# Kernel tuning notes

Measured on AMD Instinct MI355X. Metric: run time of the kernel, lower is better.

## Reference

```python
import jax, jax.numpy as jnp
import numpy as np

N_NODES = 100000
N_EDGES = 1600000
IN_CH = 128
HID = 128
OUT_CH = 64
N_GRAPHS = 256


def setup_inputs() -> dict:
    key = jax.random.key(0)
    ks = jax.random.split(key, 12)
    x = jax.random.normal(ks[0], (N_NODES, IN_CH), dtype=jnp.float32)
    edge_index = jax.random.randint(ks[1], (2, N_EDGES), 0, N_NODES, dtype=jnp.int64)
    batch = jnp.sort(jax.random.randint(ks[2], (N_NODES,), 0, N_GRAPHS, dtype=jnp.int64))
    def glorot(k, shape):
        lim = np.sqrt(6.0 / (shape[0] + shape[1]))
        return jax.random.uniform(k, shape, jnp.float32, -lim, lim)
    w1 = glorot(ks[3], (IN_CH, HID)); b1 = jnp.zeros((HID,), jnp.float32)
    w2 = glorot(ks[4], (HID, HID));   b2 = jnp.zeros((HID,), jnp.float32)
    w3 = glorot(ks[5], (HID, HID));   b3 = jnp.zeros((HID,), jnp.float32)
    w_out = glorot(ks[6], (HID, OUT_CH)); b_out = jnp.zeros((OUT_CH,), jnp.float32)
    return {"x": x, "edge_index": edge_index, "batch": batch,
            "w1": w1, "b1": b1, "w2": w2, "b2": b2, "w3": w3, "b3": b3,
            "w_out": w_out, "b_out": b_out}


def reference(x, edge_index, batch, w1, b1, w2, b2, w3, b3, w_out, b_out):
    N = x.shape[0]
    # GCN normalization with added self-loops (PyG gcn_norm, symmetric):
    loop = jnp.arange(N, dtype=edge_index.dtype)
    src = jnp.concatenate([edge_index[0], loop])  # message source
    dst = jnp.concatenate([edge_index[1], loop])  # aggregate at target
    deg = jax.ops.segment_sum(jnp.ones(src.shape, jnp.float32), dst, num_segments=N)
    dinv = jax.lax.rsqrt(jnp.maximum(deg, 1.0))  # deg >= 1 due to self-loops
    norm = dinv[src] * dinv[dst]  # [E+N]

    def gcn_conv(h, w, b):
        h = h @ w  # transform first (PyG order)
        agg = jax.ops.segment_sum(norm[:, None] * h[src], dst, num_segments=N)
        return agg + b

    # norm module is None, dropout p=0 -> act-only branch, dropout no-op
    h = jax.nn.relu(gcn_conv(x, w1, b1))
    h = jax.nn.relu(gcn_conv(h, w2, b2))
    h = jax.nn.relu(gcn_conv(h, w3, b3))

    # global mean pool over graphs
    cnt = jax.ops.segment_sum(jnp.ones((N,), jnp.float32), batch, num_segments=N_GRAPHS)
    pooled = jax.ops.segment_sum(h, batch, num_segments=N_GRAPHS) / jnp.maximum(cnt, 1.0)[:, None]
    return pooled @ w_out + b_out  # [N_GRAPHS, OUT_CH]
```

## Files before the change

### kernel.cpp

```cpp
#include <hip/hip_runtime.h>
#include <hip/hip_fp16.h>

#define N_NODES 100000
#define N_EDGES 1600000
#define HID 128
#define OUT_CH 64
#define N_GRAPHS 256
#define CHUNK 1024
#define NCHUNK ((N_NODES + CHUNK - 1) / CHUNK)
#define NSLICE 8
#define SLICE_NODES ((N_NODES + NSLICE - 1) / NSLICE)
#define CAPB 262144
#define EPW2 1600

typedef _Float16 half8 __attribute__((ext_vector_type(8)));
typedef float f32x4 __attribute__((ext_vector_type(4)));

__global__ void k_setup(int* cnt, int* bcur, float* pooled, float* gcnt,
                        const float* __restrict__ w1, const float* __restrict__ w2,
                        const float* __restrict__ w3,
                        __half* __restrict__ wt1, __half* __restrict__ wt2,
                        __half* __restrict__ wt3) {
  int i = blockIdx.x * blockDim.x + threadIdx.x;
  int stride = gridDim.x * blockDim.x;
  for (int t = i; t < N_NODES; t += stride) cnt[t] = 0;
  for (int t = i; t < NSLICE; t += stride) bcur[t] = t * CAPB;
  for (int t = i; t < N_GRAPHS * HID; t += stride) pooled[t] = 0.f;
  for (int t = i; t < N_GRAPHS; t += stride) gcnt[t] = 0.f;
  for (int t = i; t < HID * HID; t += stride) {
    int n = t >> 7, k = t & 127;
    wt1[t] = __float2half(w1[k * HID + n]);
    wt2[t] = __float2half(w2[k * HID + n]);
    wt3[t] = __float2half(w3[k * HID + n]);
  }
}

__global__ __launch_bounds__(256) void k_part(const int* __restrict__ ei,
                                              int* __restrict__ bcur,
                                              int* __restrict__ bsrc,
                                              int* __restrict__ bdst) {
  __shared__ int hist[NSLICE], rbase[NSLICE], lcur[NSLICE];
  int tid = threadIdx.x;
  int e0 = blockIdx.x * EPW2;
  int n = min(EPW2, N_EDGES - e0);
  if (n <= 0) return;
  if (tid < NSLICE) { hist[tid] = 0; lcur[tid] = 0; }
  __syncthreads();
  for (int i = tid; i < n; i += 256)
    atomicAdd(&hist[ei[N_EDGES + e0 + i] / SLICE_NODES], 1);
  __syncthreads();
  if (tid < NSLICE) rbase[tid] = atomicAdd(&bcur[tid], hist[tid]);
  __syncthreads();
  for (int i = tid; i < n; i += 256) {
    int s = ei[e0 + i], d = ei[N_EDGES + e0 + i];
    int b = d / SLICE_NODES;
    int p = rbase[b] + atomicAdd(&lcur[b], 1);
    bsrc[p] = s;
    bdst[p] = d;
  }
}

__global__ __launch_bounds__(256) void k_count2(const int* __restrict__ bdst,
                                                const int* __restrict__ bcur,
                                                int* __restrict__ cnt) {
  int b = blockIdx.x & (NSLICE - 1);
  int base = b * CAPB;
  int sz = bcur[b] - base;
  int bi = blockIdx.x >> 3;
  int step = (gridDim.x >> 3) * 256;
  for (int i = bi * 256 + threadIdx.x; i < sz; i += step)
    atomicAdd(&cnt[bdst[base + i]], 1);
}

__global__ void k_scan1(const int* __restrict__ cnt, int* __restrict__ row_ptr,
                        int* __restrict__ chunk_sums) {
  __shared__ int s[CHUNK];
  int t = threadIdx.x;
  int gid = blockIdx.x * CHUNK + t;
  int v = (gid < N_NODES) ? cnt[gid] : 0;
  s[t] = v;
  __syncthreads();
  for (int off = 1; off < CHUNK; off <<= 1) {
    int add = (t >= off) ? s[t - off] : 0;
    __syncthreads();
    s[t] += add;
    __syncthreads();
  }
  if (gid < N_NODES) row_ptr[gid] = s[t] - v;
  if (t == CHUNK - 1) chunk_sums[blockIdx.x] = s[t];
}

__global__ void k_scan2(const int* __restrict__ chunk_sums, int* __restrict__ chunk_off) {
  __shared__ int s[128];
  int t = threadIdx.x;
  int v = (t < NCHUNK) ? chunk_sums[t] : 0;
  s[t] = v;
  __syncthreads();
  for (int off = 1; off < 128; off <<= 1) {
    int add = (t >= off) ? s[t - off] : 0;
    __syncthreads();
    s[t] += add;
    __syncthreads();
  }
  if (t < NCHUNK) chunk_off[t] = s[t] - v;
}

__global__ void k_scan3(int* __restrict__ row_ptr, const int* __restrict__ chunk_off,
                        int* __restrict__ cursor, const int* __restrict__ cnt,
                        float* __restrict__ dinv) {
  int i = blockIdx.x * blockDim.x + threadIdx.x;
  if (i < N_NODES) {
    int v = row_ptr[i] + chunk_off[i / CHUNK];
    row_ptr[i] = v;
    cursor[i] = v;
    dinv[i] = rsqrtf((float)cnt[i] + 1.0f);
  }
  if (i == 0) row_ptr[N_NODES] = N_EDGES;
}

__global__ __launch_bounds__(256) void k_fill2(const int* __restrict__ bsrc,
                                               const int* __restrict__ bdst,
                                               const int* __restrict__ bcur,
                                               int* __restrict__ cursor,
                                               int* __restrict__ E4) {
  int b = blockIdx.x & (NSLICE - 1);
  int base = b * CAPB;
  int sz = bcur[b] - base;
  int bi = blockIdx.x >> 3;
  int step = (gridDim.x >> 3) * 256;
  for (int i = bi * 256 + threadIdx.x; i < sz; i += step) {
    int d = bdst[base + i];
    int p = atomicAdd(&cursor[d], 1);
    E4[p] = bsrc[base + i];
  }
}

#define GBM 128
template <bool FP16IN>
__global__ __launch_bounds__(512) void k_gemm(const void* __restrict__ Hv,
                                              const __half* __restrict__ WT,
                                              __half* __restrict__ T) {
  __shared__ __half hs[GBM * HID];
  __shared__ __half ws[HID * HID];
  int tid = threadIdx.x;
  int m0 = blockIdx.x * GBM;

  for (int g = tid; g < GBM * 16; g += 512) {
    int r = g >> 4, kg = g & 15;
    int row = m0 + r;
    half8 h = {};
    if (row < N_NODES) {
      if constexpr (FP16IN) {
        h = *(const half8*)&((const _Float16*)Hv)[(size_t)row * HID + kg * 8];
      } else {
        const float* H = (const float*)Hv;
        float4 f0 = *(const float4*)&H[(size_t)row * HID + kg * 8];
        float4 f1 = *(const float4*)&H[(size_t)row * HID + kg * 8 + 4];
        h[0] = (_Float16)f0.x; h[1] = (_Float16)f0.y; h[2] = (_Float16)f0.z; h[3] = (_Float16)f0.w;
        h[4] = (_Float16)f1.x; h[5] = (_Float16)f1.y; h[6] = (_Float16)f1.z; h[7] = (_Float16)f1.w;
      }
    }
    int byte = (r * HID + kg * 8) * 2;
    byte ^= (r & 7) << 4;
    *(half8*)((char*)hs + byte) = h;
  }
  for (int g = tid; g < HID * 16; g += 512) {
    int n = g >> 4, kg = g & 15;
    half8 h = *(const half8*)&WT[n * HID + kg * 8];
    int byte = (n * HID + kg * 8) * 2;
    byte ^= (n & 7) << 4;
    *(half8*)((char*)ws + byte) = h;
  }
  __syncthreads();

  int w = tid >> 6, l = tid & 63;
  int r = (w << 4) + (l & 15);
  int kq = (l >> 4) << 3;
  f32x4 acc[8] = {};

  #pragma unroll
  for (int kc = 0; kc < HID; kc += 32) {
    int abyte = ((r * HID + kc + kq) * 2) ^ ((r & 7) << 4);
    half8 a = *(const half8*)((char*)hs + abyte);
    #pragma unroll
    for (int nb = 0; nb < 8; ++nb) {
      int n = nb * 16 + (l & 15);
      int bbyte = ((n * HID + kc + kq) * 2) ^ ((n & 7) << 4);
      half8 bfr = *(const half8*)((char*)ws + bbyte);
      acc[nb] = __builtin_amdgcn_mfma_f32_16x16x32_f16(a, bfr, acc[nb], 0, 0, 0);
    }
  }

  __syncthreads();
  #pragma unroll
  for (int nb = 0; nb < 8; ++nb) {
    #pragma unroll
    for (int j = 0; j < 4; ++j) {
      int rr = (w << 4) + ((l >> 4) << 2) + j;
      int cc = nb * 16 + (l & 15);
      int byte = (rr * HID + cc) * 2;
      byte ^= (rr & 7) << 4;
      *(__half*)((char*)hs + byte) = __float2half(acc[nb][j]);
    }
  }
  __syncthreads();
  for (int g = tid; g < GBM * 16; g += 512) {
    int rr = g >> 4, kg = g & 15;
    int byte = (rr * HID + kg * 8) * 2;
    byte ^= (rr & 7) << 4;
    half8 v = *(half8*)((char*)hs + byte);
    int row = m0 + rr;
    if (row < N_NODES)
      *(half8*)&((_Float16*)T)[(size_t)row * HID + kg * 8] = v;
  }
}

__device__ __forceinline__ void acc8(float* acc, uint4 v, float wt) {
  __half2 h0 = *(__half2*)&v.x, h1 = *(__half2*)&v.y;
  __half2 h2 = *(__half2*)&v.z, h3 = *(__half2*)&v.w;
  float2 f0 = __half22float2(h0), f1 = __half22float2(h1);
  float2 f2 = __half22float2(h2), f3 = __half22float2(h3);
  acc[0] += wt * f0.x; acc[1] += wt * f0.y;
  acc[2] += wt * f1.x; acc[3] += wt * f1.y;
  acc[4] += wt * f2.x; acc[5] += wt * f2.y;
  acc[6] += wt * f3.x; acc[7] += wt * f3.y;
}

__global__ __launch_bounds__(256) void k_agg(const __half* __restrict__ T,
                                             const int* __restrict__ row_ptr,
                                             const int* __restrict__ E4,
                                             const float* __restrict__ dinv,
                                             const float* __restrict__ bias,
                                             __half* __restrict__ Hout) {
  int wid = (blockIdx.x * blockDim.x + threadIdx.x) >> 6;
  int lane = threadIdx.x & 63;
  if (wid >= N_NODES) return;
  int q = lane >> 4;
  int wch = lane & 15;

  float acc[8] = {};
  float dn = dinv[wid];
  {
    uint4 vs = *(const uint4*)(T + (size_t)wid * HID + wch * 8);
    acc8(acc, vs, (q == 0) ? dn * dn : 0.f);
  }
  int p0 = row_ptr[wid], p1 = row_ptr[wid + 1];
  for (int p = p0; p < p1; p += 16) {
    int i0 = p + q, i1 = p + 4 + q, i2 = p + 8 + q, i3 = p + 12 + q;
    int c0 = min(i0, p1 - 1), c1 = min(i1, p1 - 1);
    int c2 = min(i2, p1 - 1), c3 = min(i3, p1 - 1);
    int s0 = E4[c0], s1 = E4[c1], s2 = E4[c2], s3 = E4[c3];
    uint4 v0 = *(const uint4*)(T + (size_t)s0 * HID + wch * 8);
    uint4 v1 = *(const uint4*)(T + (size_t)s1 * HID + wch * 8);
    uint4 v2 = *(const uint4*)(T + (size_t)s2 * HID + wch * 8);
    uint4 v3 = *(const uint4*)(T + (size_t)s3 * HID + wch * 8);
    float w0 = (i0 < p1) ? dinv[s0] * dn : 0.f;
    float w1 = (i1 < p1) ? dinv[s1] * dn : 0.f;
    float w2 = (i2 < p1) ? dinv[s2] * dn : 0.f;
    float w3 = (i3 < p1) ? dinv[s3] * dn : 0.f;
    acc8(acc, v0, w0);
    acc8(acc, v1, w1);
    acc8(acc, v2, w2);
    acc8(acc, v3, w3);
  }
  #pragma unroll
  for (int j = 0; j < 8; ++j) {
    acc[j] += __shfl_xor(acc[j], 16, 64);
    acc[j] += __shfl_xor(acc[j], 32, 64);
  }
  if (q == 0) {
    float4 b0 = *(const float4*)(bias + wch * 8);
    float4 b1 = *(const float4*)(bias + wch * 8 + 4);
    __half2 o0 = __floats2half2_rn(fmaxf(acc[0] + b0.x, 0.f), fmaxf(acc[1] + b0.y, 0.f));
    __half2 o1 = __floats2half2_rn(fmaxf(acc[2] + b0.z, 0.f), fmaxf(acc[3] + b0.w, 0.f));
    __half2 o2 = __floats2half2_rn(fmaxf(acc[4] + b1.x, 0.f), fmaxf(acc[5] + b1.y, 0.f));
    __half2 o3 = __floats2half2_rn(fmaxf(acc[6] + b1.z, 0.f), fmaxf(acc[7] + b1.w, 0.f));
    uint4 o;
    o.x = *(unsigned int*)&o0; o.y = *(unsigned int*)&o1;
    o.z = *(unsigned int*)&o2; o.w = *(unsigned int*)&o3;
    *(uint4*)(Hout + (size_t)wid * HID + wch * 8) = o;
  }
}

#define POOL_NODES 64
__global__ __launch_bounds__(256) void k_pool(const __half* __restrict__ H,
                                              const int* __restrict__ batch,
                                              float* __restrict__ pooled,
                                              float* __restrict__ gcnt) {
  int w = threadIdx.x >> 6;
  int l = threadIdx.x & 63;
  int n0 = blockIdx.x * POOL_NODES + w * 16;
  if (n0 >= N_NODES) return;
  int n1 = min(n0 + 16, N_NODES);
  const __half2* H2 = (const __half2*)H;
  float sx = 0.f, sy = 0.f, cntr = 0.f;
  int cur = batch[n0];
  for (int n = n0; n < n1; ++n) {
    int g = batch[n];
    if (g != cur) {
      atomicAdd(&pooled[cur * HID + 2 * l], sx);
      atomicAdd(&pooled[cur * HID + 2 * l + 1], sy);
      if (l == 0) atomicAdd(&gcnt[cur], cntr);
      sx = 0.f; sy = 0.f; cntr = 0.f; cur = g;
    }
    float2 f = __half22float2(H2[(size_t)n * 64 + l]);
    sx += f.x; sy += f.y; cntr += 1.f;
  }
  atomicAdd(&pooled[cur * HID + 2 * l], sx);
  atomicAdd(&pooled[cur * HID + 2 * l + 1], sy);
  if (l == 0) atomicAdd(&gcnt[cur], cntr);
}

__global__ __launch_bounds__(64) void k_out(const float* __restrict__ pooled,
                                            const float* __restrict__ gcnt,
                                            const float* __restrict__ w_out,
                                            const float* __restrict__ b_out,
                                            float* __restrict__ out) {
  int g = blockIdx.x;
  int c = threadIdx.x;
  __shared__ float p[HID];
  float inv = 1.0f / fmaxf(gcnt[g], 1.0f);
  for (int k = c; k < HID; k += 64) p[k] = pooled[g * HID + k] * inv;
  __syncthreads();
  float acc = b_out[c];
  #pragma unroll 8
  for (int k = 0; k < HID; ++k) acc += p[k] * w_out[k * OUT_CH + c];
  out[g * OUT_CH + c] = acc;
}

extern "C" void kernel_launch(void* const* d_in, const int* in_sizes, int n_in,
                              void* d_out, int out_size, void* d_ws, size_t ws_size,
                              hipStream_t stream) {
  const float* x     = (const float*)d_in[0];
  const int*   ei    = (const int*)d_in[1];
  const int*   batch = (const int*)d_in[2];
  const float* w1    = (const float*)d_in[3];
  const float* b1    = (const float*)d_in[4];
  const float* w2    = (const float*)d_in[5];
  const float* b2    = (const float*)d_in[6];
  const float* w3    = (const float*)d_in[7];
  const float* b3    = (const float*)d_in[8];
  const float* w_out = (const float*)d_in[9];
  const float* b_out = (const float*)d_in[10];
  float* out = (float*)d_out;

  char* w = (char*)d_ws;
  auto alloc = [&](size_t bytes) { void* p = (void*)w; w += (bytes + 255) & ~(size_t)255; return p; };
  int*   cnt        = (int*)  alloc((size_t)N_NODES * 4);
  int*   row_ptr    = (int*)  alloc((size_t)(N_NODES + 1) * 4);
  int*   cursor     = (int*)  alloc((size_t)N_NODES * 4);
  float* dinv       = (float*)alloc((size_t)N_NODES * 4);
  int*   chunk_sums = (int*)  alloc((size_t)NCHUNK * 4);
  int*   chunk_off  = (int*)  alloc((size_t)NCHUNK * 4);
  int*   bcur       = (int*)  alloc((size_t)NSLICE * 4);
  int*   bsrc       = (int*)  alloc((size_t)NSLICE * CAPB * 4);
  int*   bdst       = (int*)  alloc((size_t)NSLICE * CAPB * 4);
  int*   E4         = (int*)  alloc((size_t)N_EDGES * 4);
  __half* wt1       = (__half*)alloc((size_t)HID * HID * 2);
  __half* wt2       = (__half*)alloc((size_t)HID * HID * 2);
  __half* wt3       = (__half*)alloc((size_t)HID * HID * 2);
  __half* T         = (__half*)alloc((size_t)N_NODES * HID * 2);
  __half* Hh        = (__half*)alloc((size_t)N_NODES * HID * 2);
  float* pooled     = (float*)alloc((size_t)N_GRAPHS * HID * 4);
  float* gcnt       = (float*)alloc((size_t)N_GRAPHS * 4);

  const int NB = (N_NODES + 255) / 256;
  const int GB = (N_NODES + GBM - 1) / GBM;
  const int AB = (N_NODES + 3) / 4;
  const int PB = (N_NODES + POOL_NODES - 1) / POOL_NODES;
  const int PARTB = (N_EDGES + EPW2 - 1) / EPW2;

  k_setup<<<256, 256, 0, stream>>>(cnt, bcur, pooled, gcnt, w1, w2, w3, wt1, wt2, wt3);
  k_part<<<PARTB, 256, 0, stream>>>(ei, bcur, bsrc, bdst);
  k_count2<<<2048, 256, 0, stream>>>(bdst, bcur, cnt);
  k_scan1<<<NCHUNK, CHUNK, 0, stream>>>(cnt, row_ptr, chunk_sums);
  k_scan2<<<1, 128, 0, stream>>>(chunk_sums, chunk_off);
  k_scan3<<<NB, 256, 0, stream>>>(row_ptr, chunk_off, cursor, cnt, dinv);
  k_fill2<<<2048, 256, 0, stream>>>(bsrc, bdst, bcur, cursor, E4);

  k_gemm<false><<<GB, 512, 0, stream>>>(x, wt1, T);
  k_agg<<<AB, 256, 0, stream>>>(T, row_ptr, E4, dinv, b1, Hh);
  k_gemm<true><<<GB, 512, 0, stream>>>(Hh, wt2, T);
  k_agg<<<AB, 256, 0, stream>>>(T, row_ptr, E4, dinv, b2, Hh);
  k_gemm<true><<<GB, 512, 0, stream>>>(Hh, wt3, T);
  k_agg<<<AB, 256, 0, stream>>>(T, row_ptr, E4, dinv, b3, Hh);

  k_pool<<<PB, 256, 0, stream>>>(Hh, batch, pooled, gcnt);
  k_out<<<N_GRAPHS, 64, 0, stream>>>(pooled, gcnt, w_out, b_out, out);
}
```

Baseline: 449.5 us.

## Fuse GCN aggregation and GEMM into one per-layer kernel using aggregate-then-transform order

Each GCN layer now aggregates neighbor features first (A·H) into shared memory and then multiplies by W with MFMA in the same kernel, applying bias and ReLU before writing out. This removes the intermediate T buffer round trip and one launch per layer. The input x is converted to fp16 in the setup kernel instead of inside the first GEMM. In exchange, the gather now runs with 512-thread blocks that each do 16 nodes per wave sequentially. The weight fragments are read straight from global memory instead of being staged in LDS. Aggregating before transforming also changes the floating-point rounding order.

```diff
diff --git a/kernel.cpp b/kernel.cpp
--- a/kernel.cpp
+++ b/kernel.cpp
@@ -20,7 +20,8 @@
                         const float* __restrict__ w1, const float* __restrict__ w2,
                         const float* __restrict__ w3,
                         __half* __restrict__ wt1, __half* __restrict__ wt2,
-                        __half* __restrict__ wt3) {
+                        __half* __restrict__ wt3,
+                        const float* __restrict__ x, __half* __restrict__ Xh) {
   int i = blockIdx.x * blockDim.x + threadIdx.x;
   int stride = gridDim.x * blockDim.x;
   for (int t = i; t < N_NODES; t += stride) cnt[t] = 0;
@@ -32,6 +33,15 @@
     wt1[t] = __float2half(w1[k * HID + n]);
     wt2[t] = __float2half(w2[k * HID + n]);
     wt3[t] = __float2half(w3[k * HID + n]);
+  }
+  for (int t = i; t < N_NODES * 16; t += stride) {
+    int row = t >> 4, kg = t & 15;
+    float4 f0 = *(const float4*)&x[(size_t)row * HID + kg * 8];
+    float4 f1 = *(const float4*)&x[(size_t)row * HID + kg * 8 + 4];
+    half8 h;
+    h[0] = (_Float16)f0.x; h[1] = (_Float16)f0.y; h[2] = (_Float16)f0.z; h[3] = (_Float16)f0.w;
+    h[4] = (_Float16)f1.x; h[5] = (_Float16)f1.y; h[6] = (_Float16)f1.z; h[7] = (_Float16)f1.w;
+    *(half8*)&((_Float16*)Xh)[(size_t)row * HID + kg * 8] = h;
   }
 }
 
@@ -136,85 +146,6 @@
 }
 
 #define GBM 128
-template <bool FP16IN>
-__global__ __launch_bounds__(512) void k_gemm(const void* __restrict__ Hv,
-                                              const __half* __restrict__ WT,
-                                              __half* __restrict__ T) {
-  __shared__ __half hs[GBM * HID];
-  __shared__ __half ws[HID * HID];
-  int tid = threadIdx.x;
-  int m0 = blockIdx.x * GBM;
-
-  for (int g = tid; g < GBM * 16; g += 512) {
-    int r = g >> 4, kg = g & 15;
-    int row = m0 + r;
-    half8 h = {};
-    if (row < N_NODES) {
-      if constexpr (FP16IN) {
-        h = *(const half8*)&((const _Float16*)Hv)[(size_t)row * HID + kg * 8];
-      } else {
-        const float* H = (const float*)Hv;
-        float4 f0 = *(const float4*)&H[(size_t)row * HID + kg * 8];
-        float4 f1 = *(const float4*)&H[(size_t)row * HID + kg * 8 + 4];
-        h[0] = (_Float16)f0.x; h[1] = (_Float16)f0.y; h[2] = (_Float16)f0.z; h[3] = (_Float16)f0.w;
-        h[4] = (_Float16)f1.x; h[5] = (_Float16)f1.y; h[6] = (_Float16)f1.z; h[7] = (_Float16)f1.w;
-      }
-    }
-    int byte = (r * HID + kg * 8) * 2;
-    byte ^= (r & 7) << 4;
-    *(half8*)((char*)hs + byte) = h;
-  }
-  for (int g = tid; g < HID * 16; g += 512) {
-    int n = g >> 4, kg = g & 15;
-    half8 h = *(const half8*)&WT[n * HID + kg * 8];
-    int byte = (n * HID + kg * 8) * 2;
-    byte ^= (n & 7) << 4;
-    *(half8*)((char*)ws + byte) = h;
-  }
-  __syncthreads();
-
-  int w = tid >> 6, l = tid & 63;
-  int r = (w << 4) + (l & 15);
-  int kq = (l >> 4) << 3;
-  f32x4 acc[8] = {};
-
-  #pragma unroll
-  for (int kc = 0; kc < HID; kc += 32) {
-    int abyte = ((r * HID + kc + kq) * 2) ^ ((r & 7) << 4);
-    half8 a = *(const half8*)((char*)hs + abyte);
-    #pragma unroll
-    for (int nb = 0; nb < 8; ++nb) {
-      int n = nb * 16 + (l & 15);
-      int bbyte = ((n * HID + kc + kq) * 2) ^ ((n & 7) << 4);
-      half8 bfr = *(const half8*)((char*)ws + bbyte);
-      acc[nb] = __builtin_amdgcn_mfma_f32_16x16x32_f16(a, bfr, acc[nb], 0, 0, 0);
-    }
-  }
-
-  __syncthreads();
-  #pragma unroll
-  for (int nb = 0; nb < 8; ++nb) {
-    #pragma unroll
-    for (int j = 0; j < 4; ++j) {
-      int rr = (w << 4) + ((l >> 4) << 2) + j;
-      int cc = nb * 16 + (l & 15);
-      int byte = (rr * HID + cc) * 2;
-      byte ^= (rr & 7) << 4;
-      *(__half*)((char*)hs + byte) = __float2half(acc[nb][j]);
-    }
-  }
-  __syncthreads();
-  for (int g = tid; g < GBM * 16; g += 512) {
-    int rr = g >> 4, kg = g & 15;
-    int byte = (rr * HID + kg * 8) * 2;
-    byte ^= (rr & 7) << 4;
-    half8 v = *(half8*)((char*)hs + byte);
-    int row = m0 + rr;
-    if (row < N_NODES)
-      *(half8*)&((_Float16*)T)[(size_t)row * HID + kg * 8] = v;
-  }
-}
-
 __device__ __forceinline__ void acc8(float* acc, uint4 v, float wt) {
   __half2 h0 = *(__half2*)&v.x, h1 = *(__half2*)&v.y;
   __half2 h2 = *(__half2*)&v.z, h3 = *(__half2*)&v.w;
@@ -226,59 +157,95 @@
   acc[6] += wt * f3.x; acc[7] += wt * f3.y;
 }
 
-__global__ __launch_bounds__(256) void k_agg(const __half* __restrict__ T,
-                                             const int* __restrict__ row_ptr,
-                                             const int* __restrict__ E4,
-                                             const float* __restrict__ dinv,
-                                             const float* __restrict__ bias,
-                                             __half* __restrict__ Hout) {
-  int wid = (blockIdx.x * blockDim.x + threadIdx.x) >> 6;
-  int lane = threadIdx.x & 63;
-  if (wid >= N_NODES) return;
-  int q = lane >> 4;
-  int wch = lane & 15;
-
-  float acc[8] = {};
-  float dn = dinv[wid];
-  {
-    uint4 vs = *(const uint4*)(T + (size_t)wid * HID + wch * 8);
-    acc8(acc, vs, (q == 0) ? dn * dn : 0.f);
-  }
-  int p0 = row_ptr[wid], p1 = row_ptr[wid + 1];
-  for (int p = p0; p < p1; p += 16) {
-    int i0 = p + q, i1 = p + 4 + q, i2 = p + 8 + q, i3 = p + 12 + q;
-    int c0 = min(i0, p1 - 1), c1 = min(i1, p1 - 1);
-    int c2 = min(i2, p1 - 1), c3 = min(i3, p1 - 1);
-    int s0 = E4[c0], s1 = E4[c1], s2 = E4[c2], s3 = E4[c3];
-    uint4 v0 = *(const uint4*)(T + (size_t)s0 * HID + wch * 8);
-    uint4 v1 = *(const uint4*)(T + (size_t)s1 * HID + wch * 8);
-    uint4 v2 = *(const uint4*)(T + (size_t)s2 * HID + wch * 8);
-    uint4 v3 = *(const uint4*)(T + (size_t)s3 * HID + wch * 8);
-    float w0 = (i0 < p1) ? dinv[s0] * dn : 0.f;
-    float w1 = (i1 < p1) ? dinv[s1] * dn : 0.f;
-    float w2 = (i2 < p1) ? dinv[s2] * dn : 0.f;
-    float w3 = (i3 < p1) ? dinv[s3] * dn : 0.f;
-    acc8(acc, v0, w0);
-    acc8(acc, v1, w1);
-    acc8(acc, v2, w2);
-    acc8(acc, v3, w3);
-  }
+__global__ __launch_bounds__(512) void k_layer(const __half* __restrict__ Hin,
+                                               const __half* __restrict__ WT,
+                                               const int* __restrict__ row_ptr,
+                                               const int* __restrict__ E4,
+                                               const float* __restrict__ dinv,
+                                               const float* __restrict__ bias,
+                                               __half* __restrict__ Hout) {
+  __shared__ __half hs[GBM * HID];
+  int tid = threadIdx.x;
+  int w = tid >> 6, l = tid & 63;
+  int q = l >> 4, wch = l & 15;
+  int m0 = blockIdx.x * GBM;
+
+  for (int t = 0; t < 16; ++t) {
+    int r = (w << 4) + t;
+    int node = m0 + r;
+    float acc[8] = {};
+    if (node < N_NODES) {
+      float dn = dinv[node];
+      uint4 vs = *(const uint4*)(Hin + (size_t)node * HID + wch * 8);
+      acc8(acc, vs, (q == 0) ? dn * dn : 0.f);
+      int p0 = row_ptr[node], p1 = row_ptr[node + 1];
+      for (int p = p0; p < p1; p += 16) {
+        int i0 = p + q, i1 = p + 4 + q, i2 = p + 8 + q, i3 = p + 12 + q;
+        int c0 = min(i0, p1 - 1), c1 = min(i1, p1 - 1);
+        int c2 = min(i2, p1 - 1), c3 = min(i3, p1 - 1);
+        int s0 = E4[c0], s1 = E4[c1], s2 = E4[c2], s3 = E4[c3];
+        uint4 v0 = *(const uint4*)(Hin + (size_t)s0 * HID + wch * 8);
+        uint4 v1 = *(const uint4*)(Hin + (size_t)s1 * HID + wch * 8);
+        uint4 v2 = *(const uint4*)(Hin + (size_t)s2 * HID + wch * 8);
+        uint4 v3 = *(const uint4*)(Hin + (size_t)s3 * HID + wch * 8);
+        float w0 = (i0 < p1) ? dinv[s0] * dn : 0.f;
+        float w1 = (i1 < p1) ? dinv[s1] * dn : 0.f;
+        float w2 = (i2 < p1) ? dinv[s2] * dn : 0.f;
+        float w3 = (i3 < p1) ? dinv[s3] * dn : 0.f;
+        acc8(acc, v0, w0);
+        acc8(acc, v1, w1);
+        acc8(acc, v2, w2);
+        acc8(acc, v3, w3);
+      }
+      #pragma unroll
+      for (int j = 0; j < 8; ++j) {
+        acc[j] += __shfl_xor(acc[j], 16, 64);
+        acc[j] += __shfl_xor(acc[j], 32, 64);
+      }
+    }
+    if (q == 0) {
+      half8 z;
+      #pragma unroll
+      for (int j = 0; j < 8; ++j) z[j] = (_Float16)acc[j];
+      int byte = ((r * HID + wch * 8) * 2) ^ ((r & 7) << 4);
+      *(half8*)((char*)hs + byte) = z;
+    }
+  }
+
+  int rr = (w << 4) + (l & 15);
+  int kq = (l >> 4) << 3;
+  f32x4 acc2[8] = {};
   #pragma unroll
-  for (int j = 0; j < 8; ++j) {
-    acc[j] += __shfl_xor(acc[j], 16, 64);
-    acc[j] += __shfl_xor(acc[j], 32, 64);
-  }
-  if (q == 0) {
-    float4 b0 = *(const float4*)(bias + wch * 8);
-    float4 b1 = *(const float4*)(bias + wch * 8 + 4);
-    __half2 o0 = __floats2half2_rn(fmaxf(acc[0] + b0.x, 0.f), fmaxf(acc[1] + b0.y, 0.f));
-    __half2 o1 = __floats2half2_rn(fmaxf(acc[2] + b0.z, 0.f), fmaxf(acc[3] + b0.w, 0.f));
-    __half2 o2 = __floats2half2_rn(fmaxf(acc[4] + b1.x, 0.f), fmaxf(acc[5] + b1.y, 0.f));
-    __half2 o3 = __floats2half2_rn(fmaxf(acc[6] + b1.z, 0.f), fmaxf(acc[7] + b1.w, 0.f));
-    uint4 o;
-    o.x = *(unsigned int*)&o0; o.y = *(unsigned int*)&o1;
-    o.z = *(unsigned int*)&o2; o.w = *(unsigned int*)&o3;
-    *(uint4*)(Hout + (size_t)wid * HID + wch * 8) = o;
+  for (int kc = 0; kc < HID; kc += 32) {
+    int abyte = ((rr * HID + kc + kq) * 2) ^ ((rr & 7) << 4);
+    half8 a = *(const half8*)((char*)hs + abyte);
+    #pragma unroll
+    for (int nb = 0; nb < 8; ++nb) {
+      int n = nb * 16 + (l & 15);
+      half8 bfr = *(const half8*)&WT[n * HID + kc + kq];
+      acc2[nb] = __builtin_amdgcn_mfma_f32_16x16x32_f16(a, bfr, acc2[nb], 0, 0, 0);
+    }
+  }
+
+  #pragma unroll
+  for (int nb = 0; nb < 8; ++nb) {
+    #pragma unroll
+    for (int j = 0; j < 4; ++j) {
+      int orow = (w << 4) + ((l >> 4) << 2) + j;
+      int cc = nb * 16 + (l & 15);
+      float v = fmaxf(acc2[nb][j] + bias[cc], 0.f);
+      int byte = ((orow * HID + cc) * 2) ^ ((orow & 7) << 4);
+      *(__half*)((char*)hs + byte) = __float2half(v);
+    }
+  }
+  __syncthreads();
+  for (int g = tid; g < GBM * 16; g += 512) {
+    int r2 = g >> 4, kg = g & 15;
+    int byte = ((r2 * HID + kg * 8) * 2) ^ ((r2 & 7) << 4);
+    half8 v = *(half8*)((char*)hs + byte);
+    int row = m0 + r2;
+    if (row < N_NODES)
+      *(half8*)&((_Float16*)Hout)[(size_t)row * HID + kg * 8] = v;
   }
 }
 
@@ -359,18 +326,18 @@
   __half* wt1       = (__half*)alloc((size_t)HID * HID * 2);
   __half* wt2       = (__half*)alloc((size_t)HID * HID * 2);
   __half* wt3       = (__half*)alloc((size_t)HID * HID * 2);
-  __half* T         = (__half*)alloc((size_t)N_NODES * HID * 2);
-  __half* Hh        = (__half*)alloc((size_t)N_NODES * HID * 2);
+  __half* Xh        = (__half*)alloc((size_t)N_NODES * HID * 2);
+  __half* Ha        = (__half*)alloc((size_t)N_NODES * HID * 2);
   float* pooled     = (float*)alloc((size_t)N_GRAPHS * HID * 4);
   float* gcnt       = (float*)alloc((size_t)N_GRAPHS * 4);
 
   const int NB = (N_NODES + 255) / 256;
-  const int GB = (N_NODES + GBM - 1) / GBM;
-  const int AB = (N_NODES + 3) / 4;
+  const int LB = (N_NODES + GBM - 1) / GBM;
   const int PB = (N_NODES + POOL_NODES - 1) / POOL_NODES;
   const int PARTB = (N_EDGES + EPW2 - 1) / EPW2;
 
-  k_setup<<<256, 256, 0, stream>>>(cnt, bcur, pooled, gcnt, w1, w2, w3, wt1, wt2, wt3);
+  k_setup<<<256, 256, 0, stream>>>(cnt, bcur, pooled, gcnt, w1, w2, w3,
+                                   wt1, wt2, wt3, x, Xh);
   k_part<<<PARTB, 256, 0, stream>>>(ei, bcur, bsrc, bdst);
   k_count2<<<2048, 256, 0, stream>>>(bdst, bcur, cnt);
   k_scan1<<<NCHUNK, CHUNK, 0, stream>>>(cnt, row_ptr, chunk_sums);
@@ -378,13 +345,10 @@
   k_scan3<<<NB, 256, 0, stream>>>(row_ptr, chunk_off, cursor, cnt, dinv);
   k_fill2<<<2048, 256, 0, stream>>>(bsrc, bdst, bcur, cursor, E4);
 
-  k_gemm<false><<<GB, 512, 0, stream>>>(x, wt1, T);
-  k_agg<<<AB, 256, 0, stream>>>(T, row_ptr, E4, dinv, b1, Hh);
-  k_gemm<true><<<GB, 512, 0, stream>>>(Hh, wt2, T);
-  k_agg<<<AB, 256, 0, stream>>>(T, row_ptr, E4, dinv, b2, Hh);
-  k_gemm<true><<<GB, 512, 0, stream>>>(Hh, wt3, T);
-  k_agg<<<AB, 256, 0, stream>>>(T, row_ptr, E4, dinv, b3, Hh);
-
-  k_pool<<<PB, 256, 0, stream>>>(Hh, batch, pooled, gcnt);
+  k_layer<<<LB, 512, 0, stream>>>(Xh, wt1, row_ptr, E4, dinv, b1, Ha);
+  k_layer<<<LB, 512, 0, stream>>>(Ha, wt2, row_ptr, E4, dinv, b2, Xh);
+  k_layer<<<LB, 512, 0, stream>>>(Xh, wt3, row_ptr, E4, dinv, b3, Ha);
+
+  k_pool<<<PB, 256, 0, stream>>>(Ha, batch, pooled, gcnt);
   k_out<<<N_GRAPHS, 64, 0, stream>>>(pooled, gcnt, w_out, b_out, out);
 }
```

New measurement: 571.2 us. 27.1% more time.
